# Kernel optimization log

Measured on AMD Instinct MI355X. Metric: run time of the kernel, lower is better.

Reference implementation:

```python
import jax, jax.numpy as jnp
import numpy as np

H = 200          # GRU hidden size (hard-coded in module)
D = 300          # embed_dim
V = 50000        # embed_num (vocab)
DOC_TRUNC = 10
N_DOCS = 256
T = 50           # words per sentence


def _p(k, shape):
    return jax.random.normal(k, shape, dtype=jnp.float32) * 0.05


def setup_inputs():
    key = jax.random.key(0)
    ks = jax.random.split(key, 24)
    x = jax.random.randint(ks[0], (N_DOCS * DOC_TRUNC, T), 0, V, dtype=jnp.int32)
    doc_lens = jax.random.randint(ks[1], (N_DOCS,), 0, DOC_TRUNC + 1, dtype=jnp.int32)
    emb = _p(ks[2], (V, D)).at[0].set(0.0)  # padding_idx=0 row is zero
    inp = dict(
        x=x, doc_nums=N_DOCS, doc_lens=doc_lens, emb=emb,
        wf_ih=_p(ks[3], (3 * H, D)), wf_hh=_p(ks[4], (3 * H, H)), wf_bi=_p(ks[5], (3 * H,)), wf_bh=_p(ks[6], (3 * H,)),
        wb_ih=_p(ks[7], (3 * H, D)), wb_hh=_p(ks[8], (3 * H, H)), wb_bi=_p(ks[9], (3 * H,)), wb_bh=_p(ks[10], (3 * H,)),
        sf_ih=_p(ks[11], (3 * H, 2 * H)), sf_hh=_p(ks[12], (3 * H, H)), sf_bi=_p(ks[13], (3 * H,)), sf_bh=_p(ks[14], (3 * H,)),
        sb_ih=_p(ks[15], (3 * H, 2 * H)), sb_hh=_p(ks[16], (3 * H, H)), sb_bi=_p(ks[17], (3 * H,)), sb_bh=_p(ks[18], (3 * H,)),
        doc_w=_p(ks[19], (1, 2 * H)), doc_b=_p(ks[20], (1,)),
        sent_w=_p(ks[21], (DOC_TRUNC, 2 * H)), sent_b=_p(ks[22], (DOC_TRUNC,)),
    )
    return inp


def _gru_dir(xseq, w_ih, w_hh, b_ih, b_hh, reverse=False):
    # xseq: [B, T, Din] -> outputs [B, T, H], torch GRU gate order (r, z, n)
    if reverse:
        xseq = xseq[:, ::-1]
    gx = jnp.einsum('btd,gd->btg', xseq, w_ih) + b_ih  # [B, T, 3H]
    gx = jnp.moveaxis(gx, 1, 0)                        # [T, B, 3H]
    h0 = jnp.zeros((xseq.shape[0], H), xseq.dtype)

    def step(h, gxt):
        gh = h @ w_hh.T + b_hh
        xr, xz, xn = jnp.split(gxt, 3, axis=-1)
        hr, hz, hn = jnp.split(gh, 3, axis=-1)
        r = jax.nn.sigmoid(xr + hr)
        z = jax.nn.sigmoid(xz + hz)
        n = jnp.tanh(xn + r * hn)
        h_new = (1.0 - z) * n + z * h
        return h_new, h_new

    _, hs = jax.lax.scan(step, h0, gx)
    hs = jnp.moveaxis(hs, 0, 1)  # [B, T, H]
    if reverse:
        hs = hs[:, ::-1]
    return hs


def _bigru(xseq, fw, bw):
    return jnp.concatenate([_gru_dir(xseq, *fw), _gru_dir(xseq, *bw, reverse=True)], axis=-1)


def _avg_pool(xseq, lens):
    # Faithful to max_pool1d helper: avg over first lens[i] timesteps, zeros if len==0.
    Tn = xseq.shape[1]
    mask = (jnp.arange(Tn)[None, :] < lens[:, None]).astype(xseq.dtype)  # [B, T]
    s = jnp.einsum('btf,bt->bf', xseq, mask)
    denom = jnp.maximum(lens, 1).astype(xseq.dtype)[:, None]
    return jnp.where((lens == 0)[:, None], jnp.zeros_like(s), s / denom)


def reference(x, doc_nums, doc_lens, emb,
              wf_ih, wf_hh, wf_bi, wf_bh, wb_ih, wb_hh, wb_bi, wb_bh,
              sf_ih, sf_hh, sf_bi, sf_bh, sb_ih, sb_hh, sb_bi, sb_bh,
              doc_w, doc_b, sent_w, sent_b):
    sent_lens = jnp.sum(jnp.sign(x), axis=1)                 # [B_sent]
    e = emb[x]                                               # [B_sent, T, D]
    hw = _bigru(e, (wf_ih, wf_hh, wf_bi, wf_bh), (wb_ih, wb_hh, wb_bi, wb_bh))  # [B_sent, T, 2H]
    s = _avg_pool(hw, sent_lens)                             # [B_sent, 2H]
    s = s.reshape(-1, DOC_TRUNC, 2 * H)                      # [N_docs, doc_trunc, 2H]
    hs = _bigru(s, (sf_ih, sf_hh, sf_bi, sf_bh), (sb_ih, sb_hh, sb_bi, sb_bh))  # [N_docs, doc_trunc, 2H]
    d = _avg_pool(hs, doc_lens)                              # [N_docs, 2H]
    doc_pro = (d @ doc_w.T + doc_b).reshape(-1)              # [N_docs]
    sent_pro = d @ sent_w.T + sent_b                         # [N_docs, doc_trunc]
    dl = np.asarray(doc_lens)                                # concrete index data (static)
    rows = np.repeat(np.arange(dl.shape[0]), dl)
    cols = np.concatenate([np.arange(int(l)) for l in dl]).astype(np.int32) if rows.size else np.zeros((0,), np.int32)
    target = jnp.concatenate([doc_pro, sent_pro[rows, cols]])
    return jax.nn.sigmoid(target)
```

## Files before the change

kernel.cpp:

```cpp
#include <hip/hip_runtime.h>
#include <hip/hip_bf16.h>


typedef __hip_bfloat16 bf16;
typedef _Float16 h16x8 __attribute__((ext_vector_type(8)));
typedef __fp16 fp16x2 __attribute__((ext_vector_type(2)));
typedef float f32x4 __attribute__((ext_vector_type(4)));

#define HDIM 200
#define NS   2560
#define TW   50
#define ND   256
#define DTR  10
#define VEMB 50000

#define GT   13
#define NT   39
#define NTP  40
#define KCH  7
#define HSTR 232
#define KC_W 10
#define KC_S 13

__device__ __forceinline__ float sigf(float x) {
    return __builtin_amdgcn_rcpf(1.f + __expf(-x));
}
__device__ __forceinline__ float tanh_fast(float x) {
    float e = __expf(2.f * x);
    return (e - 1.f) * __builtin_amdgcn_rcpf(e + 1.f);
}
__device__ __forceinline__ unsigned short f2h(float x) {
    union { _Float16 h; unsigned short u; } v;
    v.h = (_Float16)x;
    return v.u;
}
__device__ __forceinline__ float h2f(unsigned short u) {
    union { _Float16 h; unsigned short u; } v;
    v.u = u;
    return (float)v.h;
}
__device__ __forceinline__ unsigned pk2h(float a, float b) {
    union { fp16x2 p; unsigned u; } v;
    v.p = __builtin_amdgcn_cvt_pkrtz(a, b);
    return v.u;
}
__device__ __forceinline__ float hfsel(uint2 v, int rg) {
    unsigned u = (rg & 2) ? v.y : v.x;
    return h2f((unsigned short)((rg & 1) ? (u >> 16) : (u & 0xFFFFu)));
}

#define PB_EMBH 12500
#define PB_WHH  (PB_EMBH + 273)
#define PB_BIH  (PB_WHH + 460)
#define PB_ALL  (PB_BIH + 20)

__global__ void prepack_all(
    const float* __restrict__ emb, unsigned short* __restrict__ embH,
    const float* __restrict__ whh0, const float* __restrict__ whh1,
    const float* __restrict__ whh2, const float* __restrict__ whh3,
    unsigned short* __restrict__ Bhh,
    const float* __restrict__ wih0, const float* __restrict__ wih1,
    const float* __restrict__ wih2, const float* __restrict__ wih3,
    unsigned short* __restrict__ BiW0, unsigned short* __restrict__ BiW1,
    unsigned short* __restrict__ BiS0, unsigned short* __restrict__ BiS1,
    const int* __restrict__ x, int* __restrict__ sl,
    const float* bi0, const float* bh0, const float* bi1, const float* bh1,
    const float* bi2, const float* bh2, const float* bi3, const float* bh3,
    float* __restrict__ bt)
{
    const int b = blockIdx.x;
    const int tid = threadIdx.x;

    if (b < PB_EMBH) {
        int gid = b * 256 + tid;
        int row = gid >> 6, c = gid & 63;
        if (c >= 40) return;
        int k0 = c * 8;
        unsigned short vals[8] __attribute__((aligned(16)));
        if (k0 + 7 < 300) {
            const float4 f0 = *reinterpret_cast<const float4*>(emb + (size_t)row * 300 + k0);
            const float4 f1 = *reinterpret_cast<const float4*>(emb + (size_t)row * 300 + k0 + 4);
            unsigned u0 = pk2h(f0.x, f0.y), u1 = pk2h(f0.z, f0.w);
            unsigned u2 = pk2h(f1.x, f1.y), u3 = pk2h(f1.z, f1.w);
            vals[0] = (unsigned short)u0; vals[1] = (unsigned short)(u0 >> 16);
            vals[2] = (unsigned short)u1; vals[3] = (unsigned short)(u1 >> 16);
            vals[4] = (unsigned short)u2; vals[5] = (unsigned short)(u2 >> 16);
            vals[6] = (unsigned short)u3; vals[7] = (unsigned short)(u3 >> 16);
        } else {
#pragma unroll
            for (int jj = 0; jj < 8; ++jj) {
                int k = k0 + jj;
                vals[jj] = (k < 300) ? f2h(emb[(size_t)row * 300 + k]) : (unsigned short)0;
            }
        }
        *reinterpret_cast<uint4*>(embH + (size_t)row * 320 + k0) =
            *reinterpret_cast<const uint4*>(vals);
        return;
    }

    if (b < PB_WHH) {
        int gid = (b - PB_EMBH) * 256 + tid;
        if (gid >= 4 * NT * KCH * 64) return;
        int lane = gid & 63;
        int f = gid >> 6;
        int kc = f % KCH;
        int tIdx = (f / KCH) % NT;
        int d = f / (KCH * NT);
        const float* w = (d == 0) ? whh0 : (d == 1) ? whh1 : (d == 2) ? whh2 : whh3;
        int g = tIdx / GT, j = tIdx % GT;
        int il = j * 16 + (lane & 15);
        int n = g * HDIM + il;
        int kb = kc * 32 + (lane >> 4) * 8;
        unsigned short vals[8] __attribute__((aligned(16)));
#pragma unroll
        for (int jj = 0; jj < 8; ++jj) {
            int k = kb + jj;
            float v = (il < HDIM && k < HDIM) ? w[n * HDIM + k] : 0.f;
            vals[jj] = f2h(v);
        }
        *reinterpret_cast<float4*>(reinterpret_cast<char*>(Bhh) + (size_t)gid * 16) =
            *reinterpret_cast<const float4*>(vals);
        return;
    }

    if (b < PB_BIH) {
        int rel = b - PB_WHH;
        const float* w; unsigned short* Bp; int Kin, KC, base;
        if (rel < 100)      { w = wih0; Bp = BiW0; Kin = 300; KC = KC_W; base = 0; }
        else if (rel < 200) { w = wih1; Bp = BiW1; Kin = 300; KC = KC_W; base = 100; }
        else if (rel < 330) { w = wih2; Bp = BiS0; Kin = 400; KC = KC_S; base = 200; }
        else                { w = wih3; Bp = BiS1; Kin = 400; KC = KC_S; base = 330; }
        int gid = (rel - base) * 256 + tid;
        if (gid >= NTP * KC * 64) return;
        int lane = gid & 63;
        int f = gid >> 6;
        int kc = f % KC;
        int tIdx = f / KC;
        int g = tIdx / GT, j = tIdx % GT;
        int il = j * 16 + (lane & 15);
        int n = g * HDIM + il;
        int kb = kc * 32 + (lane >> 4) * 8;
        unsigned short vals[8] __attribute__((aligned(16)));
#pragma unroll
        for (int jj = 0; jj < 8; ++jj) {
            int k = kb + jj;
            float v = (tIdx < NT && il < HDIM && k < Kin) ? w[n * Kin + k] : 0.f;
            vals[jj] = f2h(v);
        }
        *reinterpret_cast<float4*>(reinterpret_cast<char*>(Bp) + (size_t)gid * 16) =
            *reinterpret_cast<const float4*>(vals);
        return;
    }

    {
        int gid = (b - PB_BIH) * 256 + tid;
        if (gid < NS) {
            int c = 0;
            for (int t = 0; t < TW; ++t) c += (x[gid * TW + t] != 0) ? 1 : 0;
            sl[gid] = c;
            return;
        }
        int g2 = gid - NS;
        if (g2 >= 4 * 624) return;
        int d = g2 / 624, col = g2 % 624;
        int g = col / 208, i = col % 208;
        const float* bi = (d == 0) ? bi0 : (d == 1) ? bi1 : (d == 2) ? bi2 : bi3;
        const float* bh = (d == 0) ? bh0 : (d == 1) ? bh1 : (d == 2) ? bh2 : bh3;
        float v = 0.f;
        if (i < HDIM) v = (g < 2) ? (bi[g * HDIM + i] + bh[g * HDIM + i]) : bi[2 * HDIM + i];
        bt[g2] = v;
    }
}

__global__ __launch_bounds__(512, 4) void gemm_word(
    const unsigned short* __restrict__ embH, const int* __restrict__ idx,
    const unsigned short* __restrict__ Bp,
    const float* __restrict__ bt, unsigned short* __restrict__ gxOut)
{
    __shared__ __align__(16) unsigned short As[64 * 320];

    const int tid = threadIdx.x;
    const int n_w = tid >> 6, lane = tid & 63;
    const int bm = blockIdx.x;

    {
        const int srow = tid >> 3, q8 = tid & 7;
        int rp = bm * 64 + srow;
        int tok = idx[(rp % NS) * TW + (rp / NS)];
        const unsigned short* src = embH + (size_t)tok * 320;
        const int rx = srow & 7;
        unsigned short* dst = &As[srow * 320];
#pragma unroll
        for (int jj = 0; jj < 5; ++jj) {
            int c = q8 + jj * 8;
            uint4 v = *reinterpret_cast<const uint4*>(src + c * 8);
            int slot = c ^ rx;
            *reinterpret_cast<uint4*>(dst + slot * 8) = v;
        }
    }
    __syncthreads();

    f32x4 acc[4][5];
#pragma unroll
    for (int i = 0; i < 4; ++i)
#pragma unroll
        for (int j = 0; j < 5; ++j) acc[i][j] = (f32x4){0.f, 0.f, 0.f, 0.f};

    const uint4* bq = reinterpret_cast<const uint4*>(Bp);
    const int q = lane >> 4, r15 = lane & 15;
    const int sx = r15 & 7;

#pragma unroll 2
    for (int kc = 0; kc < KC_W; ++kc) {
        h16x8 ah[4];
        const int slot = (kc * 4 + q) ^ sx;
#pragma unroll
        for (int mt = 0; mt < 4; ++mt)
            ah[mt] = *reinterpret_cast<const h16x8*>(
                &As[(mt * 16 + r15) * 320 + slot * 8]);
        uint4 b[5];
#pragma unroll
        for (int j = 0; j < 5; ++j) {
            int gnt = n_w * 5 + j;
            b[j] = bq[(size_t)(gnt * KC_W + kc) * 64 + lane];
        }
#pragma unroll
        for (int mt = 0; mt < 4; ++mt)
#pragma unroll
            for (int j = 0; j < 5; ++j)
                acc[mt][j] = __builtin_amdgcn_mfma_f32_16x16x32_f16(
                    ah[mt], *reinterpret_cast<const h16x8*>(&b[j]),
                    acc[mt][j], 0, 0, 0);
    }

    float btv[5];
#pragma unroll
    for (int j = 0; j < 5; ++j) {
        int gnt = n_w * 5 + j;
        btv[j] = (gnt < NT) ? bt[gnt * 16 + r15] : 0.f;
    }

#pragma unroll
    for (int mt = 0; mt < 4; ++mt) {
        int gmt = bm * 4 + mt;
#pragma unroll
        for (int j = 0; j < 5; ++j) {
            int gnt = n_w * 5 + j;
            if (gnt < NT) {
                uint2 v;
                v.x = pk2h(acc[mt][j][0] + btv[j], acc[mt][j][1] + btv[j]);
                v.y = pk2h(acc[mt][j][2] + btv[j], acc[mt][j][3] + btv[j]);
                *reinterpret_cast<uint2*>(reinterpret_cast<char*>(gxOut) +
                    ((size_t)(gmt * NT + gnt) * 64 + lane) * 8) = v;
            }
        }
    }
}

__global__ __launch_bounds__(512, 2) void gemm_sent(
    const float* __restrict__ Afl, int astride,
    const unsigned short* __restrict__ Bp0, const unsigned short* __restrict__ Bp1,
    const float* __restrict__ bt0, const float* __restrict__ bt1,
    unsigned short* __restrict__ gx0, unsigned short* __restrict__ gx1, int nF)
{
    __shared__ __align__(16) unsigned short As[2][128 * 32];

    const int tid = threadIdx.x;
    const int wv = tid >> 6, lane = tid & 63;
    const int d = (blockIdx.x >= nF) ? 1 : 0;
    const int bm = d ? (blockIdx.x - nF) : blockIdx.x;
    const unsigned short* Bp = d ? Bp1 : Bp0;
    const float* bt = d ? bt1 : bt0;
    unsigned short* gxOut = d ? gx1 : gx0;
    const int m_w = wv & 1, n_w = wv >> 1;

    int aaddr[4];
#pragma unroll
    for (int mt = 0; mt < 4; ++mt) {
        int row = m_w * 64 + mt * 16 + (lane & 15);
        aaddr[mt] = row * 32 + (((lane >> 4) ^ ((row >> 1) & 3)) << 3);
    }

    const int srow = tid >> 2, qk = tid & 3;
    const int ssw = (srow >> 1) & 3;

    f32x4 acc[4][10];
#pragma unroll
    for (int i = 0; i < 4; ++i)
#pragma unroll
        for (int j = 0; j < 10; ++j) acc[i][j] = (f32x4){0.f, 0.f, 0.f, 0.f};

    const uint4* bq = reinterpret_cast<const uint4*>(Bp);
    const float* arow = Afl + (size_t)(bm * 128 + srow) * astride + qk * 8;

    float4 f[2], fn[2];
#pragma unroll
    for (int j = 0; j < 2; ++j)
        f[j] = *reinterpret_cast<const float4*>(arow + j * 4);

    for (int kc = 0; kc < KC_S; ++kc) {
        unsigned short* Ab = &As[kc & 1][0];
        {
            uint4 vh;
            vh.x = pk2h(f[0].x, f[0].y);
            vh.y = pk2h(f[0].z, f[0].w);
            vh.z = pk2h(f[1].x, f[1].y);
            vh.w = pk2h(f[1].z, f[1].w);
            int slot = qk ^ ssw;
            *reinterpret_cast<uint4*>(&Ab[srow * 32 + slot * 8]) = vh;
        }
        __syncthreads();

        if (kc + 1 < KC_S) {
#pragma unroll
            for (int j = 0; j < 2; ++j)
                fn[j] = *reinterpret_cast<const float4*>(arow + (kc + 1) * 32 + j * 4);
        }

        h16x8 ah[4];
#pragma unroll
        for (int mt = 0; mt < 4; ++mt)
            ah[mt] = *reinterpret_cast<const h16x8*>(&Ab[aaddr[mt]]);

#pragma unroll
        for (int half = 0; half < 2; ++half) {
            uint4 b[5];
#pragma unroll
            for (int j = 0; j < 5; ++j) {
                int gnt = n_w * 10 + half * 5 + j;
                b[j] = bq[(size_t)(gnt * KC_S + kc) * 64 + lane];
            }
#pragma unroll
            for (int mt = 0; mt < 4; ++mt)
#pragma unroll
                for (int j = 0; j < 5; ++j)
                    acc[mt][half * 5 + j] = __builtin_amdgcn_mfma_f32_16x16x32_f16(
                        ah[mt], *reinterpret_cast<const h16x8*>(&b[j]),
                        acc[mt][half * 5 + j], 0, 0, 0);
        }
        if (kc + 1 < KC_S) { f[0] = fn[0]; f[1] = fn[1]; }
    }

    float btv[10];
#pragma unroll
    for (int j = 0; j < 10; ++j) {
        int gnt = n_w * 10 + j;
        btv[j] = (gnt < NT) ? bt[gnt * 16 + (lane & 15)] : 0.f;
    }

#pragma unroll
    for (int mt = 0; mt < 4; ++mt) {
        int gmt = bm * 8 + m_w * 4 + mt;
#pragma unroll
        for (int j = 0; j < 10; ++j) {
            int gnt = n_w * 10 + j;
            if (gnt < NT) {
                uint2 v;
                v.x = pk2h(acc[mt][j][0] + btv[j], acc[mt][j][1] + btv[j]);
                v.y = pk2h(acc[mt][j][2] + btv[j], acc[mt][j][3] + btv[j]);
                *reinterpret_cast<uint2*>(reinterpret_cast<char*>(gxOut) +
                    ((size_t)(gmt * NT + gnt) * 64 + lane) * 8) = v;
            }
        }
    }
}

__global__ __launch_bounds__(832, 4) void gru_fused(
    const unsigned short* __restrict__ gxA, const unsigned short* __restrict__ gxB,
    const unsigned short* __restrict__ Bp, int dirBase0, int dirBase1,
    const float* __restrict__ bh0, const float* __restrict__ bh1,
    const int* __restrict__ lens, float* __restrict__ pool,
    int S, int T, int poolMode, int nF)
{
    __shared__ __align__(16) unsigned short hh[2][16 * HSTR];

    const int dsel = (blockIdx.x >= nF) ? 1 : 0;
    const int lb = dsel ? (blockIdx.x - nF) : blockIdx.x;
    const unsigned short* gx = dsel ? gxB : gxA;
    const int dirBase = dsel ? dirBase1 : dirBase0;
    const float* bh = dsel ? bh1 : bh0;
    const int dirOff = dsel ? HDIM : 0;
    const int rev = dsel;

    const int tid = threadIdx.x;
    const int w = tid >> 6, lane = tid & 63;
    const int quad = lane >> 4, c = lane & 15;
    const int row0 = lb * 16;
    const int i = w * 16 + c;
    const bool iv = (i < HDIM);

    for (int p = tid; p < 16 * HSTR; p += 832) { hh[0][p] = 0; hh[1][p] = 0; }
    __syncthreads();

    const float bhn = iv ? bh[2 * HDIM + i] : 0.f;

    int slen[4];
    float hreg[4], pacc[4];
#pragma unroll
    for (int rg = 0; rg < 4; ++rg) {
        int L = lens[row0 + quad * 4 + rg];
        if (L < 0) L = 0;
        if (L > T) L = T;
        slen[rg] = L;
        hreg[rg] = 0.f; pacc[rg] = 0.f;
    }

    const float4* Bq = reinterpret_cast<const float4*>(Bp);
    h16x8 bfr[3][7];
#pragma unroll
    for (int g = 0; g < 3; ++g)
#pragma unroll
        for (int kc = 0; kc < KCH; ++kc) {
            int fidx = (dirBase + g * GT + w) * KCH + kc;
            float4 raw = Bq[(size_t)fidx * 64 + lane];
            bfr[g][kc] = *reinterpret_cast<h16x8*>(&raw);
        }

    const char* gxb = reinterpret_cast<const char*>(gx);
    const int am = c * HSTR + quad * 8;
    const int SG = S >> 4;
    const int hw0 = (quad * 4) * HSTR + i;
    const int GSTR = GT * 64 * 8;
    const int dstep = (rev ? -SG : SG) * NT * 512;
    __syncthreads();

    uint2 gxv[3], gnx[3];
    int boff;
    {
        const int t0 = rev ? (T - 1) : 0;
        boff = (((t0 * SG + lb) * NT + w) * 64 + lane) * 8;
#pragma unroll
        for (int g = 0; g < 3; ++g)
            gxv[g] = *reinterpret_cast<const uint2*>(gxb + boff + g * GSTR);
        boff += dstep;
    }

    for (int ts = 0; ts < T; ++ts) {
        const int t = rev ? (T - 1 - ts) : ts;
        const int cur = ts & 1, nxt = cur ^ 1;

        if (ts + 1 < T) {
#pragma unroll
            for (int g = 0; g < 3; ++g)
                gnx[g] = *reinterpret_cast<const uint2*>(gxb + boff + g * GSTR);
            boff += dstep;
        }

        f32x4 a0 = (f32x4){0.f, 0.f, 0.f, 0.f}, a1 = a0, a2 = a0;
#pragma unroll
        for (int kc = 0; kc < KCH; ++kc) {
            h16x8 ah = *reinterpret_cast<const h16x8*>(&hh[cur][am + kc * 32]);
            a0 = __builtin_amdgcn_mfma_f32_16x16x32_f16(ah, bfr[0][kc], a0, 0, 0, 0);
            a1 = __builtin_amdgcn_mfma_f32_16x16x32_f16(ah, bfr[1][kc], a1, 0, 0, 0);
            a2 = __builtin_amdgcn_mfma_f32_16x16x32_f16(ah, bfr[2][kc], a2, 0, 0, 0);
        }

        if (iv) {
#pragma unroll
            for (int rg = 0; rg < 4; ++rg) {
                float xr = hfsel(gxv[0], rg);
                float xz = hfsel(gxv[1], rg);
                float xn = hfsel(gxv[2], rg);
                float r = sigf(xr + a0[rg]);
                float z = sigf(xz + a1[rg]);
                float n = tanh_fast(xn + r * (a2[rg] + bhn));
                float hnew = n + z * (hreg[rg] - n);
                hreg[rg] = hnew;
                hh[nxt][hw0 + rg * HSTR] = f2h(hnew);
                pacc[rg] += (t < slen[rg]) ? hnew : 0.f;
            }
        }
        __syncthreads();
        if (ts + 1 < T) {
#pragma unroll
            for (int g = 0; g < 3; ++g) gxv[g] = gnx[g];
        }
    }

    if (iv) {
#pragma unroll
        for (int rg = 0; rg < 4; ++rg) {
            int sg = row0 + quad * 4 + rg;
            int L = slen[rg];
            float v = (L > 0) ? pacc[rg] / (float)L : 0.f;
            int prow = poolMode ? ((sg % 10) * ND + sg / 10) : sg;
            pool[(size_t)prow * 400 + dirOff + i] = v;
        }
    }
}

__global__ __launch_bounds__(64) void head_kernel(
    const float* __restrict__ d_pool, const int* __restrict__ doc_lens,
    const float* __restrict__ doc_w, const float* __restrict__ doc_b,
    const float* __restrict__ sent_w, const float* __restrict__ sent_b,
    float* __restrict__ out)
{
    const int d = blockIdx.x;
    const int lane = threadIdx.x;

    int part = 0;
#pragma unroll
    for (int rep = 0; rep < 4; ++rep) {
        int j = lane + rep * 64;
        int v = doc_lens[j];
        v = (v < 0) ? 0 : (v > DTR ? DTR : v);
        if (j < d) part += v;
    }
#pragma unroll
    for (int off = 32; off; off >>= 1) part += __shfl_down(part, off);
    int soff = __shfl(part, 0);

    int dl = doc_lens[d];
    dl = (dl < 0) ? 0 : (dl > DTR ? DTR : dl);
    const float* dv = d_pool + (size_t)d * 400;

    for (int o = 0; o <= dl; ++o) {
        const float* wrow = (o == 0) ? doc_w : sent_w + (o - 1) * 400;
        float s = 0.f;
        for (int f = lane; f < 400; f += 64) s += dv[f] * wrow[f];
#pragma unroll
        for (int off = 32; off; off >>= 1) s += __shfl_down(s, off);
        if (lane == 0) {
            float bias = (o == 0) ? doc_b[0] : sent_b[o - 1];
            out[(o == 0) ? d : (ND + soff + (o - 1))] = sigf(s + bias);
        }
    }
}

extern "C" void kernel_launch(void* const* d_in, const int* in_sizes, int n_in,
                              void* d_out, int out_size, void* d_ws, size_t ws_size,
                              hipStream_t stream) {
    const int*   x        = (const int*)d_in[0];
    const int*   doc_lens = (const int*)d_in[2];
    const float* emb      = (const float*)d_in[3];
    const float* wf_ih = (const float*)d_in[4];
    const float* wf_hh = (const float*)d_in[5];
    const float* wf_bi = (const float*)d_in[6];
    const float* wf_bh = (const float*)d_in[7];
    const float* wb_ih = (const float*)d_in[8];
    const float* wb_hh = (const float*)d_in[9];
    const float* wb_bi = (const float*)d_in[10];
    const float* wb_bh = (const float*)d_in[11];
    const float* sf_ih = (const float*)d_in[12];
    const float* sf_hh = (const float*)d_in[13];
    const float* sf_bi = (const float*)d_in[14];
    const float* sf_bh = (const float*)d_in[15];
    const float* sb_ih = (const float*)d_in[16];
    const float* sb_hh = (const float*)d_in[17];
    const float* sb_bi = (const float*)d_in[18];
    const float* sb_bh = (const float*)d_in[19];
    const float* doc_w  = (const float*)d_in[20];
    const float* doc_b  = (const float*)d_in[21];
    const float* sent_w = (const float*)d_in[22];
    const float* sent_b = (const float*)d_in[23];

    const size_t GXSZ = 159744000;
    char* ws = (char*)d_ws;
    const size_t base = GXSZ;

    unsigned short* gxF  = (unsigned short*)(ws);
    unsigned short* gxS0 = (unsigned short*)(ws);
    unsigned short* gxS1 = (unsigned short*)(ws + 8000000);
    float* s_in   = (float*)(ws + base);
    float* dpool  = (float*)(ws + base + 4096256);
    int*   sl     = (int*)(ws + base + 4096256 + 409600);
    unsigned short* Bhh  = (unsigned short*)(ws + base + 4096256 + 409600 + 10240);
    unsigned short* BiW0 = (unsigned short*)((char*)Bhh + 1118208);
    unsigned short* BiW1 = BiW0 + NTP * KC_W * 64 * 8;
    unsigned short* BiS0 = (unsigned short*)((char*)BiW0 + 819200);
    unsigned short* BiS1 = BiS0 + NTP * KC_S * 64 * 8;
    float* bt     = (float*)((char*)BiS0 + 1064960);
    unsigned short* embH = (unsigned short*)((char*)bt + 9984);

    prepack_all<<<PB_ALL, 256, 0, stream>>>(
        emb, embH,
        wf_hh, wb_hh, sf_hh, sb_hh, Bhh,
        wf_ih, wb_ih, sf_ih, sb_ih, BiW0, BiW1, BiS0, BiS1,
        x, sl,
        wf_bi, wf_bh, wb_bi, wb_bh, sf_bi, sf_bh, sb_bi, sb_bh, bt);

    gemm_word<<<2000, 512, 0, stream>>>(embH, x, BiW0, bt + 0, gxF);
    gru_fused<<<160, 832, 0, stream>>>(
        gxF, gxF, Bhh, 0 * NT, 1 * NT, wf_bh, wb_bh, sl, s_in, NS, TW, 1, 160);
    gemm_word<<<2000, 512, 0, stream>>>(embH, x, BiW1, bt + 624, gxF);
    gru_fused<<<160, 832, 0, stream>>>(
        gxF, gxF, Bhh, 0 * NT, 1 * NT, wf_bh, wb_bh, sl, s_in, NS, TW, 1, 0);

    gemm_sent<<<40, 512, 0, stream>>>(
        s_in, 400, BiS0, BiS1, bt + 2 * 624, bt + 3 * 624, gxS0, gxS1, 20);
    gru_fused<<<32, 832, 0, stream>>>(
        gxS0, gxS1, Bhh, 2 * NT, 3 * NT, sf_bh, sb_bh, doc_lens, dpool, ND, DTR, 0, 16);

    head_kernel<<<ND, 64, 0, stream>>>(dpool, doc_lens, doc_w, doc_b, sent_w, sent_b, (float*)d_out);
}
```

Baseline: 579.4 us.

## Add 7-wave word-level GRU kernel with two gate tiles per wave

Adds a word-level GRU kernel that launches 448 threads (7 waves) per block instead of 832 (13 waves). Each wave now handles two 16-column hidden tiles, holding both sets of recurrent weight fragments in registers and issuing six MFMA chains per K chunk. The word-level forward and backward launches switch to it, while the sentence-level GRU keeps the old kernel. The goal is to reuse each loaded hidden-state fragment across more MFMAs and to cut the number of waves meeting at the per-step barrier, at the cost of higher register pressure and fewer waves to hide latency.

```diff
diff --git a/kernel.cpp b/kernel.cpp
--- a/kernel.cpp
+++ b/kernel.cpp
@@ -362,6 +362,147 @@
                     ((size_t)(gmt * NT + gnt) * 64 + lane) * 8) = v;
             }
         }
+    }
+}
+
+__global__ __launch_bounds__(448, 2) void gru_word(
+    const unsigned short* __restrict__ gxA, const unsigned short* __restrict__ gxB,
+    const unsigned short* __restrict__ Bp, int dirBase0, int dirBase1,
+    const float* __restrict__ bh0, const float* __restrict__ bh1,
+    const int* __restrict__ lens, float* __restrict__ pool,
+    int S, int T, int poolMode, int nF)
+{
+    __shared__ __align__(16) unsigned short hh[2][16 * HSTR];
+
+    const int dsel = (blockIdx.x >= nF) ? 1 : 0;
+    const int lb = dsel ? (blockIdx.x - nF) : blockIdx.x;
+    const unsigned short* gx = dsel ? gxB : gxA;
+    const int dirBase = dsel ? dirBase1 : dirBase0;
+    const float* bh = dsel ? bh1 : bh0;
+    const int dirOff = dsel ? HDIM : 0;
+    const int rev = dsel;
+
+    const int tid = threadIdx.x;
+    const int w = tid >> 6, lane = tid & 63;
+    const int quad = lane >> 4, c = lane & 15;
+    const int row0 = lb * 16;
+    const int j0 = 2 * w, j1 = 2 * w + 1;
+    const int i0 = j0 * 16 + c, i1 = j1 * 16 + c;
+    const bool t1v = (j1 < GT);
+    const bool iv0 = (i0 < HDIM), iv1 = t1v && (i1 < HDIM);
+
+    for (int p = tid; p < 2 * 16 * HSTR; p += 448)
+        hh[0][p] = 0;
+    __syncthreads();
+
+    const float bhn0 = iv0 ? bh[2 * HDIM + i0] : 0.f;
+    const float bhn1 = iv1 ? bh[2 * HDIM + i1] : 0.f;
+
+    int slen[4];
+    float hr0[4], hr1[4], pa0[4], pa1[4];
+#pragma unroll
+    for (int rg = 0; rg < 4; ++rg) {
+        int L = lens[row0 + quad * 4 + rg];
+        if (L < 0) L = 0;
+        if (L > T) L = T;
+        slen[rg] = L;
+        hr0[rg] = 0.f; hr1[rg] = 0.f; pa0[rg] = 0.f; pa1[rg] = 0.f;
+    }
+
+    const float4* Bq = reinterpret_cast<const float4*>(Bp);
+    h16x8 bfr[2][3][KCH];
+#pragma unroll
+    for (int g = 0; g < 3; ++g)
+#pragma unroll
+        for (int kc = 0; kc < KCH; ++kc) {
+            {
+                int fidx = (dirBase + g * GT + j0) * KCH + kc;
+                float4 raw = Bq[(size_t)fidx * 64 + lane];
+                bfr[0][g][kc] = *reinterpret_cast<h16x8*>(&raw);
+            }
+            if (t1v) {
+                int fidx = (dirBase + g * GT + j1) * KCH + kc;
+                float4 raw = Bq[(size_t)fidx * 64 + lane];
+                bfr[1][g][kc] = *reinterpret_cast<h16x8*>(&raw);
+            }
+        }
+
+    const char* gxb = reinterpret_cast<const char*>(gx);
+    const int am = c * HSTR + quad * 8;
+    const int SG = S >> 4;
+    const int hw0 = (quad * 4) * HSTR + i0;
+    const int hw1 = (quad * 4) * HSTR + i1;
+    const int dstep = (rev ? -SG : SG) * NT * 512;
+    int boff;
+    {
+        const int t0 = rev ? (T - 1) : 0;
+        boff = ((t0 * SG + lb) * NT) * 512 + lane * 8;
+    }
+    __syncthreads();
+
+    for (int ts = 0; ts < T; ++ts) {
+        const int t = rev ? (T - 1 - ts) : ts;
+        const int cur = ts & 1, nxt = cur ^ 1;
+
+        uint2 gx0[3], gx1[3];
+#pragma unroll
+        for (int g = 0; g < 3; ++g) {
+            gx0[g] = *reinterpret_cast<const uint2*>(gxb + boff + (g * GT + j0) * 512);
+            if (t1v)
+                gx1[g] = *reinterpret_cast<const uint2*>(gxb + boff + (g * GT + j1) * 512);
+        }
+        boff += dstep;
+
+        f32x4 a00 = (f32x4){0.f, 0.f, 0.f, 0.f}, a01 = a00, a02 = a00;
+        f32x4 a10 = a00, a11 = a00, a12 = a00;
+#pragma unroll
+        for (int kc = 0; kc < KCH; ++kc) {
+            h16x8 ah = *reinterpret_cast<const h16x8*>(&hh[cur][am + kc * 32]);
+            a00 = __builtin_amdgcn_mfma_f32_16x16x32_f16(ah, bfr[0][0][kc], a00, 0, 0, 0);
+            a01 = __builtin_amdgcn_mfma_f32_16x16x32_f16(ah, bfr[0][1][kc], a01, 0, 0, 0);
+            a02 = __builtin_amdgcn_mfma_f32_16x16x32_f16(ah, bfr[0][2][kc], a02, 0, 0, 0);
+            if (t1v) {
+                a10 = __builtin_amdgcn_mfma_f32_16x16x32_f16(ah, bfr[1][0][kc], a10, 0, 0, 0);
+                a11 = __builtin_amdgcn_mfma_f32_16x16x32_f16(ah, bfr[1][1][kc], a11, 0, 0, 0);
+                a12 = __builtin_amdgcn_mfma_f32_16x16x32_f16(ah, bfr[1][2][kc], a12, 0, 0, 0);
+            }
+        }
+
+        if (iv0) {
+#pragma unroll
+            for (int rg = 0; rg < 4; ++rg) {
+                float r = sigf(hfsel(gx0[0], rg) + a00[rg]);
+                float z = sigf(hfsel(gx0[1], rg) + a01[rg]);
+                float n = tanh_fast(hfsel(gx0[2], rg) + r * (a02[rg] + bhn0));
+                float hnew = n + z * (hr0[rg] - n);
+                hr0[rg] = hnew;
+                hh[nxt][hw0 + rg * HSTR] = f2h(hnew);
+                pa0[rg] += (t < slen[rg]) ? hnew : 0.f;
+            }
+        }
+        if (iv1) {
+#pragma unroll
+            for (int rg = 0; rg < 4; ++rg) {
+                float r = sigf(hfsel(gx1[0], rg) + a10[rg]);
+                float z = sigf(hfsel(gx1[1], rg) + a11[rg]);
+                float n = tanh_fast(hfsel(gx1[2], rg) + r * (a12[rg] + bhn1));
+                float hnew = n + z * (hr1[rg] - n);
+                hr1[rg] = hnew;
+                hh[nxt][hw1 + rg * HSTR] = f2h(hnew);
+                pa1[rg] += (t < slen[rg]) ? hnew : 0.f;
+            }
+        }
+        __syncthreads();
+    }
+
+#pragma unroll
+    for (int rg = 0; rg < 4; ++rg) {
+        int sg = row0 + quad * 4 + rg;
+        int L = slen[rg];
+        int prow = poolMode ? ((sg % 10) * ND + sg / 10) : sg;
+        float inv = (L > 0) ? 1.f / (float)L : 0.f;
+        if (iv0) pool[(size_t)prow * 400 + dirOff + i0] = pa0[rg] * inv;
+        if (iv1) pool[(size_t)prow * 400 + dirOff + i1] = pa1[rg] * inv;
     }
 }
 
@@ -580,10 +721,10 @@
         wf_bi, wf_bh, wb_bi, wb_bh, sf_bi, sf_bh, sb_bi, sb_bh, bt);
 
     gemm_word<<<2000, 512, 0, stream>>>(embH, x, BiW0, bt + 0, gxF);
-    gru_fused<<<160, 832, 0, stream>>>(
+    gru_word<<<160, 448, 0, stream>>>(
         gxF, gxF, Bhh, 0 * NT, 1 * NT, wf_bh, wb_bh, sl, s_in, NS, TW, 1, 160);
     gemm_word<<<2000, 512, 0, stream>>>(embH, x, BiW1, bt + 624, gxF);
-    gru_fused<<<160, 832, 0, stream>>>(
+    gru_word<<<160, 448, 0, stream>>>(
         gxF, gxF, Bhh, 0 * NT, 1 * NT, wf_bh, wb_bh, sl, s_in, NS, TW, 1, 0);
 
     gemm_sent<<<40, 512, 0, stream>>>(
```

Result: faster. 551.5 us (-4.8%).
